# Optimization experiments

Measured on AMD Instinct MI355X. Metric: run time of the kernel, lower is better.

## Reference

```python
import jax, jax.numpy as jnp
import numpy as np

B, N, M, C, K = 4, 4096, 4096, 64, 32
RADIUS = 0.1
EPS = 1e-5


def setup_inputs() -> dict:
    key = jax.random.key(0)
    ks = jax.random.split(key, 32)
    inp = {
        "query_xyz": jax.random.uniform(ks[0], (B, N, 3), jnp.float32),
        "support_xyz": jax.random.uniform(ks[1], (B, M, 3), jnp.float32),
        "query_mask": jax.random.randint(ks[2], (B, N), 0, 2, jnp.int32),
        "support_mask": jax.random.randint(ks[3], (B, M), 0, 2, jnp.int32),
        "support_features": jax.random.normal(ks[4], (B, C, M), jnp.float32),
    }
    names = ["theta1", "theta2", "phi", "psi", "alpha", "gamma1", "gamma2"]
    in_ch = {"theta1": 3}
    for j, nm in enumerate(names):
        inp[f"W_{nm}"] = jax.random.normal(ks[5 + j], (C, in_ch.get(nm, C)), jnp.float32) * 0.05
        inp[f"b_{nm}"] = jax.random.normal(ks[12 + j], (C,), jnp.float32) * 0.05
    for j, nm in enumerate(["theta", "gamma"]):
        inp[f"g_{nm}"] = 1.0 + 0.1 * jax.random.normal(ks[19 + 2 * j], (C,), jnp.float32)
        inp[f"be_{nm}"] = 0.1 * jax.random.normal(ks[20 + 2 * j], (C,), jnp.float32)
        inp[f"rm_{nm}"] = jnp.zeros((C,), jnp.float32)
        inp[f"rv_{nm}"] = jnp.ones((C,), jnp.float32)
    return inp


def _conv(W, b, x):
    # 1x1 Conv2d: channelwise linear on [B, C_in, N, K]
    return jnp.einsum('oc,bcnk->bonk', W, x) + b[None, :, None, None]


def _bn(x, g, be, rm, rv):
    # BatchNorm2d, inference form with running stats
    inv = g / jnp.sqrt(rv + EPS)
    return x * inv[None, :, None, None] + (be - rm * inv)[None, :, None, None]


def _forward(query_xyz, support_xyz, query_mask, support_mask, support_features, P):
    Bq, Nq = query_xyz.shape[:2]
    # pairwise squared distances [B, N, M]; masked support pushed to +inf
    d2 = jnp.sum((query_xyz[:, :, None, :] - support_xyz[:, None, :, :]) ** 2, axis=-1)
    d2 = jnp.where(support_mask[:, None, :] > 0, d2, jnp.inf)
    # ball query as K-nearest-within-radius
    neg, idx = jax.lax.top_k(-d2, K)                    # idx: [B, N, K]
    nbr_mask = (-neg) <= RADIUS ** 2                    # valid-neighbor mask
    flat = idx.reshape(Bq, Nq * K)
    x_j = jnp.take_along_axis(support_features, flat[:, None, :], axis=2).reshape(Bq, -1, Nq, K)
    g_xyz = jnp.take_along_axis(support_xyz, flat[:, :, None], axis=1).reshape(Bq, Nq, K, 3)
    # normalize_xyz=True -> offsets divided by radius; layout [B, 3, N, K]
    pos = ((g_xyz - query_xyz[:, :, None, :]) / RADIUS).transpose(0, 3, 1, 2)
    # nearest-neighbor query for x_i [B, C, N]
    idx_nn = jnp.argmin(d2, axis=-1)
    x_i = jnp.take_along_axis(support_features, idx_nn[:, None, :], axis=2)
    # positional encoding delta
    delta = jax.nn.relu(_bn(_conv(P['W_theta2'], P['b_theta2'],
                                  _conv(P['W_theta1'], P['b_theta1'], pos)),
                            P['g_theta'], P['be_theta'], P['rm_theta'], P['rv_theta']))
    lin_i = _conv(P['W_phi'], P['b_phi'], x_i[..., None])   # [B,C,N,1], broadcast over K
    lin_j = _conv(P['W_psi'], P['b_psi'], x_j)
    rel = lin_i - lin_j + delta
    rel = jax.nn.relu(_bn(_conv(P['W_gamma2'], P['b_gamma2'],
                                _conv(P['W_gamma1'], P['b_gamma1'], rel)),
                          P['g_gamma'], P['be_gamma'], P['rm_gamma'], P['rv_gamma']))
    weights = jax.nn.softmax(rel, axis=-1)                   # softmax over neighbor axis
    feats = _conv(P['W_alpha'], P['b_alpha'], x_j) + delta
    fmask = nbr_mask.astype(feats.dtype) + (1.0 - query_mask.astype(feats.dtype))[:, :, None]
    feats = feats * fmask[:, None, :, :]
    return jnp.sum(weights * feats, axis=-1)                 # [B, C, N]


def reference(query_xyz, support_xyz, query_mask, support_mask, support_features,
              W_theta1, b_theta1, W_theta2, b_theta2, W_phi, b_phi, W_psi, b_psi,
              W_alpha, b_alpha, W_gamma1, b_gamma1, W_gamma2, b_gamma2,
              g_theta, be_theta, rm_theta, rv_theta, g_gamma, be_gamma, rm_gamma, rv_gamma):
    P = dict(locals())
    return _forward(query_xyz, support_xyz, query_mask, support_mask, support_features, P)
```

## Files before the change

kernel.cpp:

```cpp
#include <hip/hip_runtime.h>
#include <cstdint>
#include <cstddef>

#define NN 4096
#define MM 4096
#define CC 64
#define KK 32
#define INF_F __builtin_huge_valf()

#define SC 2304
#define CCAP 2560
#define NBUCK 256

typedef __bf16 bf16x8 __attribute__((ext_vector_type(8)));
typedef __bf16 bf16x4 __attribute__((ext_vector_type(4)));
typedef float f32x16 __attribute__((ext_vector_type(16)));

#define NFRAG 40
#define ASTRIDE 68
#define ESTRIDE 36

#define WFENCE() asm volatile("s_waitcnt lgkmcnt(0)" ::: "memory")


__device__ __forceinline__ f32x16 zero16() {
  f32x16 z;
#pragma unroll
  for (int i = 0; i < 16; ++i) z[i] = 0.0f;
  return z;
}

__device__ __forceinline__ void conv1g(const bf16x8* __restrict__ Wf, int conv, int lane,
                                       const bf16x8* B4, f32x16& a0, f32x16& a1) {
#pragma unroll
  for (int s = 0; s < 4; ++s) {
    const bf16x8 w0 = Wf[((conv * 2 + 0) * 4 + s) * 64 + lane];
    const bf16x8 w1 = Wf[((conv * 2 + 1) * 4 + s) * 64 + lane];
    a0 = __builtin_amdgcn_mfma_f32_32x32x16_bf16(w0, B4[s], a0, 0, 0, 0);
    a1 = __builtin_amdgcn_mfma_f32_32x32x16_bf16(w1, B4[s], a1, 0, 0, 0);
  }
}

__device__ __forceinline__ void sort64(float& v, int& i, int lane) {
#pragma unroll
  for (int k = 2; k <= 64; k <<= 1) {
#pragma unroll
    for (int j = k >> 1; j > 0; j >>= 1) {
      const float ov = __shfl_xor(v, j);
      const int oi = __shfl_xor(i, j);
      const bool up = ((lane & k) == 0);
      const bool lower = ((lane & j) == 0);
      const bool take = (up == lower) ? (ov < v) : (ov > v);
      if (take) { v = ov; i = oi; }
    }
  }
}

__device__ __forceinline__ void insert_cands(float vv, int ii, float& sv, int& si,
                                             float& cmax, int lane) {
  unsigned long long cand = __ballot(vv < cmax);
  while (cand) {
    const int src = __ffsll((unsigned long long)cand) - 1;
    cand &= cand - 1;
    const float dc = __shfl(vv, src);
    if (dc < cmax) {
      const int im = __shfl(ii, src);
      const float up_s = __shfl_up(sv, 1);
      const int up_i = __shfl_up(si, 1);
      const bool pg = sv > dc;
      const bool pgu = (lane > 0) && (up_s > dc);
      const float ns = pg ? (pgu ? up_s : dc) : sv;
      const int ni = pg ? (pgu ? up_i : im) : si;
      if (lane < 32) { sv = ns; si = ni; }
      cmax = __shfl(sv, 31);
    }
  }
}

__global__ void pt_setup(const float* __restrict__ sf, const float* __restrict__ sxyz,
                         const int* __restrict__ smask,
                         const float* __restrict__ Wpsi, const float* __restrict__ W2,
                         const float* __restrict__ Wg1, const float* __restrict__ Wg2,
                         const float* __restrict__ Wa, const float* __restrict__ Wphi,
                         const float* __restrict__ gT, const float* __restrict__ beT,
                         const float* __restrict__ rmT, const float* __restrict__ rvT,
                         const float* __restrict__ gG, const float* __restrict__ beG,
                         const float* __restrict__ rmG, const float* __restrict__ rvG,
                         const float* __restrict__ b2, const float* __restrict__ bg1,
                         const float* __restrict__ bg2, const float* __restrict__ ba,
                         __bf16* __restrict__ ftb, float4* __restrict__ sx4,
                         __bf16* __restrict__ Wpack, float* __restrict__ WphiT,
                         float4* __restrict__ eo, float4* __restrict__ bo,
                         int* __restrict__ cnt2) {
  const int blk = blockIdx.x;
  const int tid = threadIdx.x;

  if (blk < 256) {
    const int b = blk >> 6;
    const int m = ((blk & 63) << 6) + (tid & 63);
    const int cg = tid >> 6;
    float v[16];
#pragma unroll
    for (int j = 0; j < 16; ++j) v[j] = sf[((size_t)(b * CC + cg * 16 + j)) * MM + m];
    __bf16* db = ftb + ((size_t)(b * MM + m)) * CC + cg * 16;
    bf16x8 t0, t1;
#pragma unroll
    for (int j = 0; j < 8; ++j) { t0[j] = (__bf16)v[j]; t1[j] = (__bf16)v[8 + j]; }
    *(bf16x8*)db = t0;
    *(bf16x8*)(db + 8) = t1;
    if (cg == 0) {
      const size_t g = (size_t)(b * MM + m);
      sx4[g] = make_float4(sxyz[g * 3 + 0], sxyz[g * 3 + 1], sxyz[g * 3 + 2], 0.0f);
    }
    return;
  }

  if (blk < 320) {
    __shared__ int hcnt[NBUCK];
    const int sub = blk - 256;
    const int b = sub >> 4;
    const int s = sub & 15;
    hcnt[tid] = 0;
    __syncthreads();
    const int m = s * 256 + tid;
    const size_t g = (size_t)b * MM + m;
    if (smask[g] > 0) {
      int bk = (int)(sxyz[g * 3 + 0] * 256.0f);
      bk = min(max(bk, 0), NBUCK - 1);
      atomicAdd(&hcnt[bk], 1);
    }
    __syncthreads();
    cnt2[(b * 16 + s) * NBUCK + tid] = hcnt[tid];
    return;
  }

  const int t = (blk - 320) * 256 + tid;
  if (t < NFRAG * 64) {
    const int lane = t & 63;
    const int fi = t >> 6;
    const int s = fi & 3;
    const int mt = (fi >> 2) & 1;
    const int conv = fi >> 3;
    const float* W = conv == 0 ? Wpsi : conv == 1 ? W2 : conv == 2 ? Wg1 : conv == 3 ? Wg2 : Wa;
    const int m = mt * 32 + (lane & 31);
    const int k0 = s * 16 + (lane >> 5) * 8;
    bf16x8 vh;
#pragma unroll
    for (int j = 0; j < 8; ++j) vh[j] = (__bf16)W[m * CC + k0 + j];
    ((bf16x8*)Wpack)[fi * 64 + lane] = vh;
    return;
  }
  const int t2 = t - NFRAG * 64;
  if (t2 < CC * CC) {
    WphiT[t2] = Wphi[(t2 & 63) * CC + (t2 >> 6)];
    return;
  }
  const int o = t2 - CC * CC;
  if (o < CC) {
    const float invT = gT[o] / sqrtf(rvT[o] + 1e-5f);
    const float invG = gG[o] / sqrtf(rvG[o] + 1e-5f);
    eo[o] = make_float4(invT, beT[o] - rmT[o] * invT, invG, beG[o] - rmG[o] * invG);
    bo[o] = make_float4(b2[o], bg1[o], bg2[o], ba[o]);
  }
}

__global__ void pt_scatter(const float* __restrict__ sxyz, const int* __restrict__ smask,
                           const int* __restrict__ cnt2, float4* __restrict__ cpts,
                           int* __restrict__ boffp) {
  __shared__ int cur[NBUCK];
  __shared__ int wtot[4];
  const int b = blockIdx.x >> 4;
  const int s = blockIdx.x & 15;
  const int tid = threadIdx.x;
  const int lane = tid & 63;
  const int w = tid >> 6;

  int c[16];
  int tot = 0;
#pragma unroll
  for (int ss = 0; ss < 16; ++ss) {
    c[ss] = cnt2[(b * 16 + ss) * NBUCK + tid];
    tot += c[ss];
  }
  int inc = tot;
#pragma unroll
  for (int off = 1; off < 64; off <<= 1) {
    const int o = __shfl_up(inc, off);
    if (lane >= off) inc += o;
  }
  if (lane == 63) wtot[w] = inc;
  __syncthreads();
  int excl = inc - tot;
#pragma unroll
  for (int i = 0; i < 4; ++i) excl += (i < w) ? wtot[i] : 0;
  const int total = wtot[0] + wtot[1] + wtot[2] + wtot[3];
  int base = excl;
#pragma unroll
  for (int ss = 0; ss < 16; ++ss) base += (ss < s) ? c[ss] : 0;
  cur[tid] = base;
  if (s == 0) {
    boffp[b * 257 + tid] = excl;
    if (tid == 0) boffp[b * 257 + 256] = total;
  }
  if (s == 15) {
    float4* dst = cpts + (size_t)b * CCAP;
    for (int i = total + tid; i < SC; i += 256)
      dst[i] = make_float4(1e4f, 1e4f, 1e4f, __int_as_float(0));
  }
  __syncthreads();
  const int m = s * 256 + tid;
  const size_t g = (size_t)b * MM + m;
  if (smask[g] > 0) {
    const float x = sxyz[g * 3 + 0];
    const float y = sxyz[g * 3 + 1];
    const float z = sxyz[g * 3 + 2];
    int bk = (int)(x * 256.0f);
    bk = min(max(bk, 0), NBUCK - 1);
    const int pos = atomicAdd(&cur[bk], 1);
    cpts[(size_t)b * CCAP + pos] = make_float4(x, y, z, __int_as_float(m));
  }
}

__global__ void pt_knn(const float* __restrict__ qxyz, const float4* __restrict__ cpts,
                       const int* __restrict__ boff, const __bf16* __restrict__ ftb,
                       const float* __restrict__ WphiT, const float* __restrict__ bphi,
                       const float* __restrict__ bpsi,
                       int* __restrict__ oidx, unsigned* __restrict__ ovalid,
                       float* __restrict__ lin) {
  const int lane = threadIdx.x & 63;
  const int qi = blockIdx.x * 4 + (threadIdx.x >> 6);
  const int b = qi >> 12;
  const float qx = qxyz[qi * 3 + 0];
  const float qy = qxyz[qi * 3 + 1];
  const float qz = qxyz[qi * 3 + 2];
  const float4* sb = cpts + (size_t)b * CCAP;
  const int* bo = boff + b * 257;
  const int cnt = bo[256];

  float R = 0.155f;
#pragma unroll
  for (int it = 0; it < 2; ++it) {
    const float cx = fminf(qx + R, 1.0f) - fmaxf(qx - R, 0.0f);
    const float cy = fminf(qy + R, 1.0f) - fmaxf(qy - R, 0.0f);
    const float cz = fminf(qz + R, 1.0f) - fmaxf(qz - R, 0.0f);
    const float n = fmaxf((float)cnt * 0.5235988f * cx * cy * cz, 1.0f);
    R *= __powf(48.0f / n, 0.33333333f);
  }
  R = fminf(fmaxf(R, 0.06f), 0.7f);

  const int lob = max((int)((qx - R) * 256.0f), 0);
  const int hib = min((int)((qx + R) * 256.0f), NBUCK - 1);
  const int r0 = bo[lob] >> 6;
  const int r1 = (bo[hib + 1] + 63) >> 6;

  float v0 = INF_F, v1 = INF_F, v2 = INF_F, v3 = INF_F;
  int i0 = 0, i1 = 0, i2 = 0, i3 = 0;
  int r = r0;
#pragma unroll 1
  for (; r + 4 <= r1; r += 4) {
    float4 P[4];
#pragma unroll
    for (int u = 0; u < 4; ++u) P[u] = sb[(r + u) * 64 + lane];
#pragma unroll
    for (int u = 0; u < 4; ++u) {
      const float dx = P[u].x - qx, dy = P[u].y - qy, dz = P[u].z - qz;
      const float d = dx * dx + dy * dy + dz * dz;
      const int m = __float_as_int(P[u].w);
      const bool c3 = d < v3, c2 = d < v2, c1 = d < v1, c0 = d < v0;
      v3 = c3 ? (c2 ? v2 : d) : v3;  i3 = c3 ? (c2 ? i2 : m) : i3;
      v2 = c2 ? (c1 ? v1 : d) : v2;  i2 = c2 ? (c1 ? i1 : m) : i2;
      v1 = c1 ? (c0 ? v0 : d) : v1;  i1 = c1 ? (c0 ? i0 : m) : i1;
      v0 = c0 ? d : v0;              i0 = c0 ? m : i0;
    }
  }
#pragma unroll 1
  for (; r < r1; ++r) {
    const float4 p = sb[r * 64 + lane];
    const float dx = p.x - qx, dy = p.y - qy, dz = p.z - qz;
    const float d = dx * dx + dy * dy + dz * dz;
    const int m = __float_as_int(p.w);
    const bool c3 = d < v3, c2 = d < v2, c1 = d < v1, c0 = d < v0;
    v3 = c3 ? (c2 ? v2 : d) : v3;  i3 = c3 ? (c2 ? i2 : m) : i3;
    v2 = c2 ? (c1 ? v1 : d) : v2;  i2 = c2 ? (c1 ? i1 : m) : i2;
    v1 = c1 ? (c0 ? v0 : d) : v1;  i1 = c1 ? (c0 ? i0 : m) : i1;
    v0 = c0 ? d : v0;              i0 = c0 ? m : i0;
  }

  float sv = v0;
  int si = i0;
  sort64(sv, si, lane);
  float cmax = __shfl(sv, 31);
  insert_cands(v1, i1, sv, si, cmax, lane);
  insert_cands(v2, i2, sv, si, cmax, lane);
  insert_cands(v3, i3, sv, si, cmax, lane);

  if (__ballot(v3 < cmax) && r1 > r0) {
    {
      const float4 p = sb[r0 * 64 + lane];
      const float dx = p.x - qx, dy = p.y - qy, dz = p.z - qz;
      float v = dx * dx + dy * dy + dz * dz;
      int id = __float_as_int(p.w);
      sort64(v, id, lane);
      sv = v; si = id;
    }
    cmax = __shfl(sv, 31);
    for (int rr = r0 + 1; rr < r1; ++rr) {
      const float4 p = sb[rr * 64 + lane];
      const float dx = p.x - qx, dy = p.y - qy, dz = p.z - qz;
      const float d = dx * dx + dy * dy + dz * dz;
      insert_cands(d, __float_as_int(p.w), sv, si, cmax, lane);
    }
  }

  const float gl = (lob > 0) ? (qx - (float)lob * 0.00390625f) : INF_F;
  const float gr = (hib < NBUCK - 1) ? ((float)(hib + 1) * 0.00390625f - qx) : INF_F;
  const float G = fminf(gl, gr);
  if (cmax > G * G) {
    const float R1 = sqrtf(cmax);
    const int lob2 = max((int)((qx - R1) * 256.0f), 0);
    const int hib2 = min((int)((qx + R1) * 256.0f), NBUCK - 1);
    const int s0 = bo[lob2] >> 6;
    const int s1 = (bo[hib2 + 1] + 63) >> 6;
    for (int rr = s0; rr < r0; ++rr) {
      const float4 p = sb[rr * 64 + lane];
      const float dx = p.x - qx, dy = p.y - qy, dz = p.z - qz;
      insert_cands(dx * dx + dy * dy + dz * dz, __float_as_int(p.w), sv, si, cmax, lane);
    }
    for (int rr = r1; rr < s1; ++rr) {
      const float4 p = sb[rr * 64 + lane];
      const float dx = p.x - qx, dy = p.y - qy, dz = p.z - qz;
      insert_cands(dx * dx + dy * dy + dz * dz, __float_as_int(p.w), sv, si, cmax, lane);
    }
  }

  if (lane < 32) oidx[(size_t)qi * KK + lane] = si;
  const unsigned long long vb = __ballot((lane < 32) && (sv <= 0.01f));
  if (lane == 0) ovalid[qi] = (unsigned)(vb & 0xffffffffull);

  const int nnb = __shfl(si, 0);
  const bf16x8* xr = (const bf16x8*)(ftb + ((size_t)(b * MM + nnb)) * CC);
  float a = bphi[lane] - bpsi[lane];
#pragma unroll
  for (int i = 0; i < 8; ++i) {
    const bf16x8 xv = xr[i];
#pragma unroll
    for (int j = 0; j < 8; ++j) a += WphiT[(8 * i + j) * CC + lane] * (float)xv[j];
  }
  lin[qi * CC + lane] = a;
}

__launch_bounds__(256, 3)
__global__ void pt_fused(
    const float* __restrict__ qxyz, const float4* __restrict__ sx4,
    const int* __restrict__ qmask, const __bf16* __restrict__ ftb,
    const int* __restrict__ kidx, const unsigned* __restrict__ kvalid,
    const float* __restrict__ lin,
    const float* __restrict__ W1, const float* __restrict__ b1,
    const __bf16* __restrict__ Wpack, const float4* __restrict__ eo,
    const float4* __restrict__ bo, float* __restrict__ out) {
  __shared__ float EPI[4][CC * ESTRIDE];
  __shared__ float4 sEO[CC], sBO[CC];
  const int wid = threadIdx.x >> 6;
  const int lane = threadIdx.x & 63;
  const int g = lane >> 5;
  const int col = lane & 31;
  const int q = blockIdx.x * 4 + wid;
  const int b = q >> 12;
  const int nq = q & (NN - 1);
  float* epi = EPI[wid];
  __bf16* act = (__bf16*)epi;
  const bf16x8* Wf = (const bf16x8*)Wpack;

  sEO[lane] = eo[lane];
  sBO[lane] = bo[lane];

  const int idx = kidx[q * KK + col];
  const float fm = (float)((kvalid[q] >> col) & 1u) + 1.0f - (float)qmask[q];

  bf16x8 Xb[4];
  {
    const __bf16* ftq = ftb + ((size_t)(b * MM + idx)) * CC;
#pragma unroll
    for (int s = 0; s < 4; ++s) Xb[s] = *(const bf16x8*)(ftq + s * 16 + g * 8);
  }

  bf16x8 Tb[4];
  {
    const float qx = qxyz[q * 3 + 0], qy = qxyz[q * 3 + 1], qz = qxyz[q * 3 + 2];
    const float4 pj = sx4[(size_t)b * MM + idx];
    const float p0 = (pj.x - qx) * 10.0f;
    const float p1 = (pj.y - qy) * 10.0f;
    const float p2 = (pj.z - qz) * 10.0f;
#pragma unroll
    for (int s = 0; s < 4; ++s) {
      bf16x8 t;
#pragma unroll
      for (int j = 0; j < 8; ++j) {
        const int c = s * 16 + g * 8 + j;
        t[j] = (__bf16)(b1[c] + W1[c * 3 + 0] * p0 + W1[c * 3 + 1] * p1 + W1[c * 3 + 2] * p2);
      }
      Tb[s] = t;
    }
  }
  WFENCE();

  float DELv[32];
  {
    f32x16 aT0 = zero16(), aT1 = zero16();
    conv1g(Wf, 1, lane, Tb, aT0, aT1);
#pragma unroll
    for (int mt = 0; mt < 2; ++mt)
#pragma unroll
      for (int t = 0; t < 4; ++t)
#pragma unroll
        for (int i = 0; i < 4; ++i) {
          const int r = t * 4 + i;
          const int o = mt * 32 + 8 * t + 4 * g + i;
          const float4 e = sEO[o];
          DELv[mt * 16 + r] = fmaxf(((mt ? aT1[r] : aT0[r]) + sBO[o].x) * e.x + e.y, 0.0f);
        }
  }

  {
    f32x16 aP0 = zero16(), aP1 = zero16();
    conv1g(Wf, 0, lane, Xb, aP0, aP1);
#pragma unroll
    for (int mt = 0; mt < 2; ++mt)
#pragma unroll
      for (int t = 0; t < 4; ++t) {
        const int ob = mt * 32 + 8 * t + 4 * g;
        const float4 lv = *(const float4*)(lin + q * CC + ob);
        const float lva[4] = {lv.x, lv.y, lv.z, lv.w};
        bf16x4 w;
#pragma unroll
        for (int i = 0; i < 4; ++i) {
          const int r = t * 4 + i;
          w[i] = (__bf16)(lva[i] - (mt ? aP1[r] : aP0[r]) + DELv[mt * 16 + r]);
        }
        *(bf16x4*)(act + col * ASTRIDE + ob) = w;
      }
  }
  WFENCE();

  {
    bf16x8 Rb[4];
#pragma unroll
    for (int s = 0; s < 4; ++s) {
      const bf16x4 lo = *(const bf16x4*)(act + col * ASTRIDE + s * 16 + g * 8);
      const bf16x4 hi = *(const bf16x4*)(act + col * ASTRIDE + s * 16 + g * 8 + 4);
      Rb[s] = bf16x8{lo[0], lo[1], lo[2], lo[3], hi[0], hi[1], hi[2], hi[3]};
    }
    f32x16 a0 = zero16(), a1 = zero16();
    conv1g(Wf, 2, lane, Rb, a0, a1);
#pragma unroll
    for (int mt = 0; mt < 2; ++mt)
#pragma unroll
      for (int t = 0; t < 4; ++t) {
        const int ob = mt * 32 + 8 * t + 4 * g;
        bf16x4 w;
#pragma unroll
        for (int i = 0; i < 4; ++i) {
          const int r = t * 4 + i;
          w[i] = (__bf16)((mt ? a1[r] : a0[r]) + sBO[ob + i].y);
        }
        *(bf16x4*)(act + col * ASTRIDE + ob) = w;
      }
  }
  WFENCE();

  f32x16 h0 = zero16(), h1 = zero16();
  {
    bf16x8 Rb[4];
#pragma unroll
    for (int s = 0; s < 4; ++s) {
      const bf16x4 lo = *(const bf16x4*)(act + col * ASTRIDE + s * 16 + g * 8);
      const bf16x4 hi = *(const bf16x4*)(act + col * ASTRIDE + s * 16 + g * 8 + 4);
      Rb[s] = bf16x8{lo[0], lo[1], lo[2], lo[3], hi[0], hi[1], hi[2], hi[3]};
    }
    conv1g(Wf, 3, lane, Rb, h0, h1);
  }
  WFENCE();

#pragma unroll
  for (int mt = 0; mt < 2; ++mt)
#pragma unroll
    for (int t = 0; t < 4; ++t)
#pragma unroll
      for (int i = 0; i < 4; ++i) {
        const int r = t * 4 + i;
        const int o = mt * 32 + 4 * g + 8 * t + i;
        const float4 e = sEO[o];
        const float v = fmaxf(((mt ? h1[r] : h0[r]) + sBO[o].z) * e.z + e.w, 0.0f);
        epi[o * ESTRIDE + col] = v;
      }
  WFENCE();

  float ev[32];
  float sum;
  {
    const float* row = epi + lane * ESTRIDE;
    float mx = -INF_F;
#pragma unroll
    for (int n = 0; n < 32; n += 4) {
      const float4 t = *(const float4*)(row + n);
      ev[n] = t.x; ev[n + 1] = t.y; ev[n + 2] = t.z; ev[n + 3] = t.w;
      mx = fmaxf(mx, fmaxf(fmaxf(t.x, t.y), fmaxf(t.z, t.w)));
    }
    sum = 0.0f;
#pragma unroll
    for (int n = 0; n < 32; ++n) { ev[n] = __expf(ev[n] - mx); sum += ev[n]; }
  }
  WFENCE();

  f32x16 fa0 = zero16(), fa1 = zero16();
  conv1g(Wf, 4, lane, Xb, fa0, fa1);

#pragma unroll
  for (int mt = 0; mt < 2; ++mt)
#pragma unroll
    for (int t = 0; t < 4; ++t)
#pragma unroll
      for (int i = 0; i < 4; ++i) {
        const int r = t * 4 + i;
        const int o = mt * 32 + 4 * g + 8 * t + i;
        const float f = ((mt ? fa1[r] : fa0[r]) + sBO[o].w + DELv[mt * 16 + r]) * fm;
        epi[o * ESTRIDE + col] = f;
      }
  WFENCE();

  {
    const float* row = epi + lane * ESTRIDE;
    float acc = 0.0f;
#pragma unroll
    for (int n = 0; n < 32; n += 4) {
      const float4 t = *(const float4*)(row + n);
      acc += ev[n] * t.x + ev[n + 1] * t.y + ev[n + 2] * t.z + ev[n + 3] * t.w;
    }
    out[((size_t)(b * CC + lane)) * NN + nq] = acc * __builtin_amdgcn_rcpf(sum);
  }
}

extern "C" void kernel_launch(void* const* d_in, const int* in_sizes, int n_in,
                              void* d_out, int out_size, void* d_ws, size_t ws_size,
                              hipStream_t stream) {
  (void)in_sizes; (void)n_in; (void)out_size; (void)ws_size;
  const float* qxyz = (const float*)d_in[0];
  const float* sxyz = (const float*)d_in[1];
  const int* qmask = (const int*)d_in[2];
  const int* smask = (const int*)d_in[3];
  const float* sfeat = (const float*)d_in[4];
  const float* W1 = (const float*)d_in[5];
  const float* b1 = (const float*)d_in[6];
  const float* W2 = (const float*)d_in[7];
  const float* b2 = (const float*)d_in[8];
  const float* Wphi = (const float*)d_in[9];
  const float* bphi = (const float*)d_in[10];
  const float* Wpsi = (const float*)d_in[11];
  const float* bpsi = (const float*)d_in[12];
  const float* Wa = (const float*)d_in[13];
  const float* ba = (const float*)d_in[14];
  const float* Wg1 = (const float*)d_in[15];
  const float* bg1 = (const float*)d_in[16];
  const float* Wg2 = (const float*)d_in[17];
  const float* bg2 = (const float*)d_in[18];
  const float* gT = (const float*)d_in[19];
  const float* beT = (const float*)d_in[20];
  const float* rmT = (const float*)d_in[21];
  const float* rvT = (const float*)d_in[22];
  const float* gG = (const float*)d_in[23];
  const float* beG = (const float*)d_in[24];
  const float* rmG = (const float*)d_in[25];
  const float* rvG = (const float*)d_in[26];

  char* ws = (char*)d_ws;
  int* kidx      = (int*)(ws + 0);
  unsigned* kval = (unsigned*)(ws + 2097152);
  __bf16* ftb    = (__bf16*)(ws + 2162688);
  float4* sx4    = (float4*)(ws + 4259840);
  float* lin     = (float*)(ws + 4521984);
  __bf16* Wpack  = (__bf16*)(ws + 8716288);
  float4* eo     = (float4*)(ws + 8757248);
  float4* bo     = (float4*)(ws + 8758272);
  float4* cpts   = (float4*)(ws + 8759296);
  float* WphiT   = (float*)(ws + 8923136);
  int* boffp     = (int*)(ws + 8939520);
  int* cnt2      = (int*)(ws + 8943744);

  hipLaunchKernelGGL(pt_setup, dim3(347), dim3(256), 0, stream,
                     sfeat, sxyz, smask,
                     Wpsi, W2, Wg1, Wg2, Wa, Wphi,
                     gT, beT, rmT, rvT, gG, beG, rmG, rvG, b2, bg1, bg2, ba,
                     ftb, sx4, Wpack, WphiT, eo, bo, cnt2);
  hipLaunchKernelGGL(pt_scatter, dim3(64), dim3(256), 0, stream,
                     sxyz, smask, cnt2, cpts, boffp);
  hipLaunchKernelGGL(pt_knn, dim3(4096), dim3(256), 0, stream,
                     qxyz, cpts, boffp, ftb, WphiT, bphi, bpsi, kidx, kval, lin);
  hipLaunchKernelGGL(pt_fused, dim3(4096), dim3(256), 0, stream,
                     qxyz, sx4, qmask, ftb, kidx, kval, lin,
                     W1, b1, Wpack, eo, bo, (float*)d_out);
}
```

Baseline: 228.8 us.

## Preload MFMA weight fragments into registers and coalesce output stores via LDS

Loads the first 24 packed weight fragments into per-lane registers at kernel start, so the first three 1x1 convolutions read weights from registers instead of issuing global loads inside each MFMA loop. Output writes now go through a small shared buffer: each block's four query results per channel are written by 64 threads as one float4 store, replacing scattered per-wave scalar stores. The memory clobber is dropped from the LDS wait fence. The trade-off is 96 extra VGPRs of weights, which may hurt occupancy under the 3-blocks launch bound, plus a new block-wide barrier before the store.

```diff
diff --git a/kernel.cpp b/kernel.cpp
--- a/kernel.cpp
+++ b/kernel.cpp
@@ -17,10 +17,11 @@
 typedef float f32x16 __attribute__((ext_vector_type(16)));
 
 #define NFRAG 40
+#define NPRE 24
 #define ASTRIDE 68
 #define ESTRIDE 36
 
-#define WFENCE() asm volatile("s_waitcnt lgkmcnt(0)" ::: "memory")
+#define WFENCE() asm volatile("s_waitcnt lgkmcnt(0)")
 
 
 __device__ __forceinline__ f32x16 zero16() {
@@ -28,6 +29,15 @@
 #pragma unroll
   for (int i = 0; i < 16; ++i) z[i] = 0.0f;
   return z;
+}
+
+__device__ __forceinline__ void conv1(const bf16x8* Wr, int conv,
+                                      const bf16x8* B4, f32x16& a0, f32x16& a1) {
+#pragma unroll
+  for (int s = 0; s < 4; ++s) {
+    a0 = __builtin_amdgcn_mfma_f32_32x32x16_bf16(Wr[(conv * 2 + 0) * 4 + s], B4[s], a0, 0, 0, 0);
+    a1 = __builtin_amdgcn_mfma_f32_32x32x16_bf16(Wr[(conv * 2 + 1) * 4 + s], B4[s], a1, 0, 0, 0);
+  }
 }
 
 __device__ __forceinline__ void conv1g(const bf16x8* __restrict__ Wf, int conv, int lane,
@@ -360,16 +370,20 @@
     const float4* __restrict__ bo, float* __restrict__ out) {
   __shared__ float EPI[4][CC * ESTRIDE];
   __shared__ float4 sEO[CC], sBO[CC];
+  __shared__ float sOUT[CC][4];
   const int wid = threadIdx.x >> 6;
   const int lane = threadIdx.x & 63;
   const int g = lane >> 5;
   const int col = lane & 31;
   const int q = blockIdx.x * 4 + wid;
   const int b = q >> 12;
-  const int nq = q & (NN - 1);
   float* epi = EPI[wid];
   __bf16* act = (__bf16*)epi;
   const bf16x8* Wf = (const bf16x8*)Wpack;
+
+  bf16x8 Wr[NPRE];
+#pragma unroll
+  for (int f = 0; f < NPRE; ++f) Wr[f] = Wf[f * 64 + lane];
 
   sEO[lane] = eo[lane];
   sBO[lane] = bo[lane];
@@ -407,7 +421,7 @@
   float DELv[32];
   {
     f32x16 aT0 = zero16(), aT1 = zero16();
-    conv1g(Wf, 1, lane, Tb, aT0, aT1);
+    conv1(Wr, 1, Tb, aT0, aT1);
 #pragma unroll
     for (int mt = 0; mt < 2; ++mt)
 #pragma unroll
@@ -423,7 +437,7 @@
 
   {
     f32x16 aP0 = zero16(), aP1 = zero16();
-    conv1g(Wf, 0, lane, Xb, aP0, aP1);
+    conv1(Wr, 0, Xb, aP0, aP1);
 #pragma unroll
     for (int mt = 0; mt < 2; ++mt)
 #pragma unroll
@@ -451,7 +465,7 @@
       Rb[s] = bf16x8{lo[0], lo[1], lo[2], lo[3], hi[0], hi[1], hi[2], hi[3]};
     }
     f32x16 a0 = zero16(), a1 = zero16();
-    conv1g(Wf, 2, lane, Rb, a0, a1);
+    conv1(Wr, 2, Rb, a0, a1);
 #pragma unroll
     for (int mt = 0; mt < 2; ++mt)
 #pragma unroll
@@ -536,7 +550,16 @@
       const float4 t = *(const float4*)(row + n);
       acc += ev[n] * t.x + ev[n + 1] * t.y + ev[n + 2] * t.z + ev[n + 3] * t.w;
     }
-    out[((size_t)(b * CC + lane)) * NN + nq] = acc * __builtin_amdgcn_rcpf(sum);
+    sOUT[lane][wid] = acc * __builtin_amdgcn_rcpf(sum);
+  }
+  __syncthreads();
+
+  if (threadIdx.x < 64) {
+    const int q0 = blockIdx.x * 4;
+    const int b0 = q0 >> 12;
+    const int nq0 = q0 & (NN - 1);
+    *(float4*)(out + ((size_t)(b0 * CC + threadIdx.x)) * NN + nq0) =
+        *(const float4*)&sOUT[threadIdx.x][0];
   }
 }
 
```

After: 225.1 us (median of 2 runs). Within noise of the previous version (-1.6%).
